# Optimization experiments

Hardware: AMD Instinct MI355X
Metric: run time of the kernel (lower is better)

## Reference

```python
import jax, jax.numpy as jnp
import numpy as np

NEG_INF = -1e30  # log-domain 'zero' (avoid -inf for numerical safety)


def ctc_loss(labels, logits, label_length, logit_length, blank_index=0):
    """Per-example CTC negative log-likelihood.

    labels:       [B, L] int, dense, padded (values != blank within label_length)
    logits:       [T, B, V] float, time-major (TF ctc_loss_v2 default)
    label_length: [B] int
    logit_length: [B] int
    returns:      [B] float, -log p(labels | logits)
    """
    T, B, V = logits.shape
    L = labels.shape[1]
    S = 2 * L + 1  # extended label sequence: blank, l1, blank, l2, ..., blank

    logp = jax.nn.log_softmax(logits, axis=-1)  # [T, B, V]

    # Extended label sequence per batch element: ext[:, 0::2] = blank, ext[:, 1::2] = labels
    ext = jnp.full((B, S), blank_index, dtype=labels.dtype)
    ext = ext.at[:, 1::2].set(labels)  # [B, S]

    # Emission log-probs for each extended position: emit[t, b, s] = logp[t, b, ext[b, s]]
    emit = jnp.take_along_axis(
        logp, jnp.broadcast_to(ext[None].astype(jnp.int32), (T, B, S)), axis=2
    )  # [T, B, S]

    # Skip transition s-2 -> s allowed iff ext[s] != blank and ext[s] != ext[s-2]
    ext_m2 = jnp.concatenate(
        [jnp.full((B, 2), -1, dtype=labels.dtype), ext[:, :-2]], axis=1
    )
    skip_ok = (ext != blank_index) & (ext != ext_m2)  # [B, S]

    def shift(a, k):
        # shift right along S by k, filling with NEG_INF
        return jnp.concatenate(
            [jnp.full((B, k), NEG_INF, dtype=a.dtype), a[:, :-k]], axis=1
        )

    # alpha at t=0: only positions 0 (blank) and 1 (first label) are reachable
    alpha0 = jnp.full((B, S), NEG_INF, dtype=logits.dtype)
    alpha0 = alpha0.at[:, 0].set(emit[0, :, 0]).at[:, 1].set(emit[0, :, 1])

    def step(alpha, xs):
        emit_t, t = xs  # emit_t: [B, S], t: scalar time index
        cand = jnp.stack(
            [alpha, shift(alpha, 1), jnp.where(skip_ok, shift(alpha, 2), NEG_INF)],
            axis=0,
        )  # [3, B, S]
        new = jax.nn.logsumexp(cand, axis=0) + emit_t
        # Freeze alpha for samples whose logit sequence has ended
        new = jnp.where((t < logit_length)[:, None], new, alpha)
        return new, None

    ts = jnp.arange(1, T)
    alpha, _ = jax.lax.scan(step, alpha0, (emit[1:], ts))  # [B, S]

    b = jnp.arange(B)
    end = 2 * label_length  # index of trailing blank for each sample
    ll = jnp.logaddexp(alpha[b, end], alpha[b, jnp.maximum(end - 1, 0)])
    return -ll  # [B]


def setup_inputs() -> dict:
    key = jax.random.key(0)
    k1, k2, k3 = jax.random.split(key, 3)
    T, B, V, L = 1024, 64, 256, 256
    logits = jax.random.normal(k1, (T, B, V), dtype=jnp.float32)
    # labels avoid the blank index (0)
    labels = jax.random.randint(k2, (B, L), 1, V, dtype=jnp.int32)
    label_length = jax.random.randint(k3, (B,), L // 2, L + 1, dtype=jnp.int32)
    logit_length = jnp.full((B,), T, dtype=jnp.int32)
    return {
        "labels": labels,
        "logits": logits,
        "label_length": label_length,
        "logit_length": logit_length,
    }


def reference(labels, logits, label_length, logit_length):
    # CTCLossEndpointCpu: loss = reduce_mean(ctc_loss_v2(...)) with blank_index=0
    per_example = ctc_loss(labels, logits, label_length, logit_length, blank_index=0)
    return jnp.mean(per_example)
```

## Files before the change

### kernel.cpp

```cpp
#include <hip/hip_runtime.h>
#include <math.h>


constexpr int V = 256;
constexpr float LN2_F = 0.6931471805599453f;

typedef unsigned uint2v __attribute__((ext_vector_type(2)));

template <int CTRL>
__device__ __forceinline__ float dpp_mov_f(float x) {
    return __int_as_float(__builtin_amdgcn_update_dpp(
        0, __float_as_int(x), CTRL, 0xF, 0xF, true));
}

__device__ __forceinline__ float wave_shr1_f(float x) {
    return __int_as_float(__builtin_amdgcn_update_dpp(
        0, __float_as_int(x), 0x138, 0xF, 0xF, true));
}

__device__ __forceinline__ float wave_max_f(float m) {
    m = fmaxf(m, dpp_mov_f<0xB1>(m));
    m = fmaxf(m, dpp_mov_f<0x4E>(m));
    m = fmaxf(m, dpp_mov_f<0x124>(m));
    m = fmaxf(m, dpp_mov_f<0x128>(m));
#if __has_builtin(__builtin_amdgcn_permlane16_swap) && __has_builtin(__builtin_amdgcn_permlane32_swap)
    uint2v a = __builtin_amdgcn_permlane16_swap(__float_as_uint(m),
                                                __float_as_uint(m), false, false);
    m = fmaxf(__uint_as_float(a.x), __uint_as_float(a.y));
    uint2v b = __builtin_amdgcn_permlane32_swap(__float_as_uint(m),
                                                __float_as_uint(m), false, false);
    m = fmaxf(__uint_as_float(b.x), __uint_as_float(b.y));
#else
    m = fmaxf(m, __shfl_xor(m, 16, 64));
    m = fmaxf(m, __shfl_xor(m, 32, 64));
#endif
    return m;
}

__device__ __forceinline__ float wave_sum_f(float s) {
    s += dpp_mov_f<0xB1>(s);
    s += dpp_mov_f<0x4E>(s);
    s += dpp_mov_f<0x124>(s);
    s += dpp_mov_f<0x128>(s);
#if __has_builtin(__builtin_amdgcn_permlane16_swap) && __has_builtin(__builtin_amdgcn_permlane32_swap)
    uint2v a = __builtin_amdgcn_permlane16_swap(__float_as_uint(s),
                                                __float_as_uint(s), false, false);
    s = __uint_as_float(a.x) + __uint_as_float(a.y);
    uint2v b = __builtin_amdgcn_permlane32_swap(__float_as_uint(s),
                                                __float_as_uint(s), false, false);
    s = __uint_as_float(b.x) + __uint_as_float(b.y);
#else
    s += __shfl_xor(s, 16, 64);
    s += __shfl_xor(s, 32, 64);
#endif
    return s;
}

#define MACS(EB, E1, E3, E5, E7) do {                                  \
    const float c7m = wave_shr1_f(cur7);                               \
    curT = (curT + cur7) * (EB);                                       \
    cur7 = fmaf(sk7, cur5, cur7 + cur6) * (E7);                        \
    cur6 = (cur6 + cur5) * (EB);                                       \
    cur5 = fmaf(sk5, cur3, cur5 + cur4) * (E5);                        \
    cur4 = (cur4 + cur3) * (EB);                                       \
    cur3 = fmaf(sk3, cur1, cur3 + cur2) * (E3);                        \
    cur2 = (cur2 + cur1) * (EB);                                       \
    cur1 = fmaf(sk1, c7m, cur1 + cur0) * (E1);                         \
    cur0 = (cur0 + c7m) * (EB);                                        \
  } while (0)

#define RENORM do {                                                    \
    curT *= mkT; cur0 *= mk0; cur1 *= mk1; cur2 *= mk2; cur3 *= mk3;   \
    cur4 *= mk4; cur5 *= mk5; cur6 *= mk6; cur7 *= mk7;                \
    float _m = fmaxf(curT, cur0); _m = fmaxf(_m, cur1);                \
    _m = fmaxf(_m, cur2); _m = fmaxf(_m, cur3); _m = fmaxf(_m, cur4);  \
    _m = fmaxf(_m, cur5); _m = fmaxf(_m, cur6); _m = fmaxf(_m, cur7);  \
    _m = wave_max_f(_m);                                               \
    const float _inv = 1.f / fmaxf(_m, 1e-30f);                        \
    log2acc -= log2f(_inv);                                            \
    curT *= _inv; cur0 *= _inv; cur1 *= _inv; cur2 *= _inv;            \
    cur3 *= _inv; cur4 *= _inv; cur5 *= _inv; cur6 *= _inv;            \
    cur7 *= _inv;                                                      \
  } while (0)

#define PRE(N, S) do {                                                 \
    G##N = *(const float4*)(&gbuf[h][S][l][0]);                        \
    A##N = bbuf[h][S];                                                 \
  } while (0)
#define STEPR(N, S) do {                                               \
    MACS(A##N, G##N.x, G##N.y, G##N.z, G##N.w);                        \
    PRE(N, S);                                                         \
  } while (0)
#define STEPC(N) MACS(A##N, G##N.x, G##N.y, G##N.z, G##N.w)

#define PLOAD(dst, WV, J)                                              \
    dst = *(const float4*)(lg + rs * (size_t)(16 * (WV) + p + 7 * (J)) + 4 * l)
#define PROC(XV, i) do {                                               \
    float4 _e;                                                         \
    _e.x = __expf((XV).x); _e.y = __expf((XV).y);                      \
    _e.z = __expf((XV).z); _e.w = __expf((XV).w);                      \
    *(float4*)&prow[p][4 * l] = _e;                                    \
    const float* _pr = prow[p];                                        \
    float _gb = _pr[0];                                                \
    float4 _gv;                                                        \
    _gv.x = _pr[ix]; _gv.y = _pr[iy]; _gv.z = _pr[iz]; _gv.w = _pr[iw];\
    *(float4*)&gbuf[h][i][l][0] = _gv;                                 \
    if (l == 0) bbuf[h][i] = _gb;                                      \
  } while (0)

#define WG_BARRIER asm volatile("s_waitcnt lgkmcnt(0)\n\ts_barrier" ::: "memory")

__global__ __launch_bounds__(512) void ctc_main(
    const int*   __restrict__ labels,
    const float* __restrict__ logits,
    const int*   __restrict__ label_len,
    const int*   __restrict__ logit_len,
    float*       __restrict__ partial,
    float*       __restrict__ lnterm,
    int T, int B, int L)
{
    const int tid = threadIdx.x;
    const int wid = tid >> 6;
    const int l   = tid & 63;

    if ((int)blockIdx.x < B) {
        __shared__ __align__(16) float gbuf[2][16][64][4];
        __shared__ float bbuf[2][16];
        __shared__ __align__(16) float prow[7][256];
        __shared__ float afin[514];

        const int b = blockIdx.x;
        const int Tb = logit_len[b];
        const int Lb = label_len[b];
        const int Sb = 2 * Lb + 1;

        const float* lg = logits + (size_t)b * V;
        const size_t rs = (size_t)B * V;

        const int4 lb4 = ((const int4*)(labels + (size_t)b * L))[l];
        const int ix = lb4.x, iy = lb4.y, iz = lb4.z, iw = lb4.w;
        const int prevw = __shfl_up(iw, 1);
        const float sk1 = (l > 0 && ix != prevw) ? 1.f : 0.f;
        const float sk3 = (iy != ix) ? 1.f : 0.f;
        const float sk5 = (iz != iy) ? 1.f : 0.f;
        const float sk7 = (iw != iz) ? 1.f : 0.f;

        const float mk0 = (8 * l + 0 < Sb) ? 1.f : 0.f;
        const float mk1 = (8 * l + 1 < Sb) ? 1.f : 0.f;
        const float mk2 = (8 * l + 2 < Sb) ? 1.f : 0.f;
        const float mk3 = (8 * l + 3 < Sb) ? 1.f : 0.f;
        const float mk4 = (8 * l + 4 < Sb) ? 1.f : 0.f;
        const float mk5 = (8 * l + 5 < Sb) ? 1.f : 0.f;
        const float mk6 = (8 * l + 6 < Sb) ? 1.f : 0.f;
        const float mk7 = (8 * l + 7 < Sb) ? 1.f : 0.f;
        const float mkT = (Sb > 512 && l == 63) ? 1.f : 0.f;

        float cur0 = 0.f, cur1 = 0.f, cur2 = 0.f, cur3 = 0.f;
        float cur4 = 0.f, cur5 = 0.f, cur6 = 0.f, cur7 = 0.f, curT = 0.f;
        if (l == 0) {
            cur0 = __expf(lg[0]);
            cur1 = __expf(lg[ix]) * mk1;
        }
        float log2acc = 0.f;

        const int NW = Tb / 16;

        float4 G0{}, G1{}, G2{}, G3{}, G4{}, G5{}, G6{}, G7{};
        float  A0 = 0, A1 = 0, A2 = 0, A3 = 0, A4 = 0, A5 = 0, A6 = 0, A7 = 0;

        const int p = (wid > 0) ? wid - 1 : 0;
        const bool three = (p < 2);
        float4 ca{}, cb{}, cc{}, na{}, nb{}, nc{};
        if (wid > 0 && NW > 0) {
            PLOAD(ca, 0, 0);
            PLOAD(cb, 0, 1);
            if (three) PLOAD(cc, 0, 2);
        }
        if (wid == 0) __builtin_amdgcn_s_setprio(1);

        for (int k = 0; k <= NW; ++k) {
            if (wid != 0) {
                if (k < NW) {
                    const int h = k & 1;
                    if (k + 1 < NW) {
                        PLOAD(na, k + 1, 0);
                        PLOAD(nb, k + 1, 1);
                        if (three) PLOAD(nc, k + 1, 2);
                    }
                    PROC(ca, p);
                    PROC(cb, p + 7);
                    if (three) PROC(cc, p + 14);
                    ca = na; cb = nb; cc = nc;
                }
            } else if (k >= 1) {
                const int w = k - 1;
                const int h = w & 1;
                if (w == 0) {
                    PRE(1, 1); PRE(2, 2); PRE(3, 3); PRE(4, 4);
                    PRE(5, 5); PRE(6, 6); PRE(7, 7); PRE(0, 8);
                    STEPR(1, 9);  STEPR(2, 10); STEPR(3, 11); STEPR(4, 12);
                    STEPR(5, 13); STEPR(6, 14); STEPR(7, 15);
                    STEPC(0);
                    STEPC(1); STEPC(2); STEPC(3); STEPC(4);
                    STEPC(5); STEPC(6); STEPC(7);
                } else {
                    PRE(0, 0); PRE(1, 1); PRE(2, 2); PRE(3, 3);
                    PRE(4, 4); PRE(5, 5); PRE(6, 6); PRE(7, 7);
                    STEPR(0, 8);  STEPR(1, 9);  STEPR(2, 10); STEPR(3, 11);
                    STEPR(4, 12); STEPR(5, 13); STEPR(6, 14); STEPR(7, 15);
                    STEPC(0); STEPC(1); STEPC(2); STEPC(3);
                    STEPC(4); STEPC(5); STEPC(6); STEPC(7);
                }
                RENORM;
            }
            WG_BARRIER;
        }

        if (wid == 0) {
            for (int t = 16 * NW; t < Tb; ++t) {
                if (t < 1) continue;
                const float* rowp = lg + rs * (size_t)t;
                const float eb = __expf(rowp[0]);
                const float e1 = __expf(rowp[ix]), e3 = __expf(rowp[iy]);
                const float e5 = __expf(rowp[iz]), e7 = __expf(rowp[iw]);
                MACS(eb, e1, e3, e5, e7);
            }

            afin[8 * l + 0] = cur0; afin[8 * l + 1] = cur1;
            afin[8 * l + 2] = cur2; afin[8 * l + 3] = cur3;
            afin[8 * l + 4] = cur4; afin[8 * l + 5] = cur5;
            afin[8 * l + 6] = cur6; afin[8 * l + 7] = cur7;
            if (l == 63) afin[512] = curT;
            const int end = 2 * Lb;
            const int em1 = (end > 0) ? end - 1 : 0;
            float ssum = afin[end] + afin[em1];
            ssum = fmaxf(ssum, 1e-37f);
            if (l == 0) lnterm[b] = logf(ssum) + LN2_F * log2acc;
        }
    } else {
        const int w  = ((int)blockIdx.x - B) * 8 + wid;
        const int nW = ((int)gridDim.x - B) * 8;
        const int rows = T * B;
        const int bb = w % B;
        const int Tbb = logit_len[bb];
        float acc = 0.f;
        int r = w;
        if (r < rows) {
            int t = w / B;
            const int ts = nW / B;
            float4 nxt = ((const float4*)(logits + (size_t)r * V))[l];
            while (true) {
                const int rn = r + nW;
                const bool more = rn < rows;
                const float4 x = nxt;
                if (more) nxt = ((const float4*)(logits + (size_t)rn * V))[l];
                float m = fmaxf(fmaxf(x.x, x.y), fmaxf(x.z, x.w));
                m = wave_max_f(m);
                float ss = __expf(x.x - m) + __expf(x.y - m) +
                           __expf(x.z - m) + __expf(x.w - m);
                ss = wave_sum_f(ss);
                if (t < Tbb) acc += m + logf(ss);
                if (!more) break;
                r = rn; t += ts;
            }
        }
        if (l == 0) partial[w] = acc;
    }
}

__global__ __launch_bounds__(64) void ctc_final(
    const float* __restrict__ partial,
    const float* __restrict__ lnterm,
    float* __restrict__ out, int B, int nW)
{
    const int b = threadIdx.x;
    float v = 0.f;
    if (b < B) {
        float c = 0.f;
        for (int k = b; k < nW; k += B) c += partial[k];
        v = c - lnterm[b];
    }
    #pragma unroll
    for (int o = 32; o >= 1; o >>= 1) v += __shfl_xor(v, o, 64);
    if (threadIdx.x == 0) out[0] = v / (float)B;
}

extern "C" void kernel_launch(void* const* d_in, const int* in_sizes, int n_in,
                              void* d_out, int out_size, void* d_ws, size_t ws_size,
                              hipStream_t stream) {
    const int*   labels    = (const int*)d_in[0];
    const float* logits    = (const float*)d_in[1];
    const int*   label_len = (const int*)d_in[2];
    const int*   logit_len = (const int*)d_in[3];

    const int B = in_sizes[2];
    const int L = in_sizes[0] / B;
    const int T = in_sizes[1] / (B * V);

    const int nLse = 1024;
    float* partial = (float*)d_ws;
    float* lnterm  = partial + nLse;

    ctc_main<<<B + nLse / 8, 512, 0, stream>>>(labels, logits, label_len,
                                               logit_len, partial, lnterm,
                                               T, B, L);
    ctc_final<<<1, 64, 0, stream>>>(partial, lnterm, (float*)d_out, B, nLse);
}
```

Before: 165.2 us.

## Split CTC into pre-gather/LSE kernel and streamlined recursion kernel

Adds a first kernel that computes per-row log-sum-exp partials and gathers exp(logit) values for each sample's labels into a contiguous workspace buffer. A second 64-thread-per-sample kernel then runs the alpha recursion, streaming from that compact buffer with deep register prefetch. It also folds the final mean into the recursion kernel using an atomic counter, removing the separate final kernel. This relies on a large workspace, with the old fused path kept as a fallback, and it adds an extra global write and read of the gathered data.

Measured after the change: 224.1 us. 35.7% more time.

```diff
diff --git a/kernel.cpp b/kernel.cpp
--- a/kernel.cpp
+++ b/kernel.cpp
@@ -82,6 +82,218 @@
     cur3 *= _inv; cur4 *= _inv; cur5 *= _inv; cur6 *= _inv;            \
     cur7 *= _inv;                                                      \
   } while (0)
+
+__global__ __launch_bounds__(256) void ctc_gather_lse(
+    const int*   __restrict__ labels,
+    const float* __restrict__ logits,
+    const int*   __restrict__ logit_len,
+    float*       __restrict__ partial,
+    float*       __restrict__ ggath,
+    float*       __restrict__ bgath,
+    int*         __restrict__ cnt,
+    int T, int B, int L)
+{
+    const int wid = threadIdx.x >> 6;
+    const int l   = threadIdx.x & 63;
+    if (blockIdx.x == 0 && threadIdx.x == 0) cnt[0] = 0;
+
+    __shared__ __align__(16) float erow[4][256];
+    float* er = erow[wid];
+
+    const int w  = (int)blockIdx.x * 4 + wid;
+    const int nW = (int)gridDim.x * 4;
+    const int rows = T * B;
+    const int bb = w % B;
+    const int Tbb = logit_len[bb];
+
+    const int4 lb4 = ((const int4*)(labels + (size_t)bb * L))[l];
+    const int ix = lb4.x, iy = lb4.y, iz = lb4.z, iw = lb4.w;
+
+    float acc = 0.f;
+    int r = w;
+    if (r < rows) {
+        int t = w / B;
+        const int ts = nW / B;
+        float4 nxt = ((const float4*)(logits + (size_t)r * V))[l];
+        while (true) {
+            const int rn = r + nW;
+            const bool more = rn < rows;
+            const float4 x = nxt;
+            if (more) nxt = ((const float4*)(logits + (size_t)rn * V))[l];
+            float4 e4;
+            e4.x = __expf(x.x); e4.y = __expf(x.y);
+            e4.z = __expf(x.z); e4.w = __expf(x.w);
+            ((float4*)er)[l] = e4;
+            float m = fmaxf(fmaxf(x.x, x.y), fmaxf(x.z, x.w));
+            m = wave_max_f(m);
+            float ss = __expf(x.x - m) + __expf(x.y - m) +
+                       __expf(x.z - m) + __expf(x.w - m);
+            ss = wave_sum_f(ss);
+            float4 g;
+            g.x = er[ix]; g.y = er[iy]; g.z = er[iz]; g.w = er[iw];
+            const float gb0 = er[0];
+            float* gr = ggath + ((size_t)bb * T + t) * 256;
+            ((float4*)gr)[l] = g;
+            if (l == 0) bgath[(size_t)bb * T + t] = gb0;
+            if (t < Tbb) acc += m + logf(ss);
+            if (!more) break;
+            r = rn; t += ts;
+        }
+    }
+    if (l == 0) partial[w] = acc;
+}
+
+#define GROWC(TROW) (*(const float4*)(gb + 256 * (size_t)((TROW) > Tm1 ? Tm1 : (TROW)) + 4 * l))
+#define BROWC(TROW) (*(const float4*)(bb_ + ((TROW) > Tm4 ? Tm4 : (TROW))))
+
+#define KSTEP(TT, SL, ABL) do {                                        \
+    MACS((ABL), R##SL.x, R##SL.y, R##SL.z, R##SL.w);                   \
+    R##SL = GROWC((TT) + 16);                                          \
+  } while (0)
+
+#define WIN16(BASE, K0, K1, K2, K3) do {                               \
+    KSTEP((BASE) +  0,  0, (K0).x); KSTEP((BASE) +  1,  1, (K0).y);    \
+    KSTEP((BASE) +  2,  2, (K0).z); KSTEP((BASE) +  3,  3, (K0).w);    \
+    K0 = BROWC((BASE) + 32);                                           \
+    KSTEP((BASE) +  4,  4, (K1).x); KSTEP((BASE) +  5,  5, (K1).y);    \
+    KSTEP((BASE) +  6,  6, (K1).z); KSTEP((BASE) +  7,  7, (K1).w);    \
+    K1 = BROWC((BASE) + 36);                                           \
+    KSTEP((BASE) +  8,  8, (K2).x); KSTEP((BASE) +  9,  9, (K2).y);    \
+    KSTEP((BASE) + 10, 10, (K2).z); KSTEP((BASE) + 11, 11, (K2).w);    \
+    K2 = BROWC((BASE) + 40);                                           \
+    KSTEP((BASE) + 12, 12, (K3).x); KSTEP((BASE) + 13, 13, (K3).y);    \
+    KSTEP((BASE) + 14, 14, (K3).z); KSTEP((BASE) + 15, 15, (K3).w);    \
+    K3 = BROWC((BASE) + 44);                                           \
+    RENORM;                                                            \
+  } while (0)
+
+#define W0FIRST() do {                                                 \
+    KSTEP( 1,  1, blkA0.y); KSTEP( 2,  2, blkA0.z); KSTEP( 3,  3, blkA0.w); \
+    blkA0 = BROWC(32);                                                 \
+    KSTEP( 4,  4, blkA1.x); KSTEP( 5,  5, blkA1.y);                    \
+    KSTEP( 6,  6, blkA1.z); KSTEP( 7,  7, blkA1.w);                    \
+    blkA1 = BROWC(36);                                                 \
+    KSTEP( 8,  8, blkA2.x); KSTEP( 9,  9, blkA2.y);                    \
+    KSTEP(10, 10, blkA2.z); KSTEP(11, 11, blkA2.w);                    \
+    blkA2 = BROWC(40);                                                 \
+    KSTEP(12, 12, blkA3.x); KSTEP(13, 13, blkA3.y);                    \
+    KSTEP(14, 14, blkA3.z); KSTEP(15, 15, blkA3.w);                    \
+    blkA3 = BROWC(44);                                                 \
+    RENORM;                                                            \
+  } while (0)
+
+__global__ __launch_bounds__(64) void ctc_rec(
+    const int*   __restrict__ labels,
+    const float* __restrict__ logits,
+    const int*   __restrict__ label_len,
+    const int*   __restrict__ logit_len,
+    const float* __restrict__ partial,
+    const float* __restrict__ ggath,
+    const float* __restrict__ bgath,
+    float*       __restrict__ vbuf,
+    int*         __restrict__ cnt,
+    float*       __restrict__ out,
+    int T, int B, int L, int nLse)
+{
+    const int l = threadIdx.x;
+    const int b = blockIdx.x;
+    __shared__ float afin[514];
+
+    const int Tb = logit_len[b];
+    const int Lb = label_len[b];
+    const int Sb = 2 * Lb + 1;
+    const int Tm1 = T - 1;
+    const int Tm4 = T - 4;
+
+    const float* lg  = logits + (size_t)b * V;
+    const size_t rs  = (size_t)B * V;
+    const float* gb  = ggath + (size_t)b * T * 256;
+    const float* bb_ = bgath + (size_t)b * T;
+
+    const int4 lb4 = ((const int4*)(labels + (size_t)b * L))[l];
+    const int ix = lb4.x, iy = lb4.y, iz = lb4.z, iw = lb4.w;
+    const int prevw = __shfl_up(iw, 1);
+    const float sk1 = (l > 0 && ix != prevw) ? 1.f : 0.f;
+    const float sk3 = (iy != ix) ? 1.f : 0.f;
+    const float sk5 = (iz != iy) ? 1.f : 0.f;
+    const float sk7 = (iw != iz) ? 1.f : 0.f;
+
+    const float mk0 = (8 * l + 0 < Sb) ? 1.f : 0.f;
+    const float mk1 = (8 * l + 1 < Sb) ? 1.f : 0.f;
+    const float mk2 = (8 * l + 2 < Sb) ? 1.f : 0.f;
+    const float mk3 = (8 * l + 3 < Sb) ? 1.f : 0.f;
+    const float mk4 = (8 * l + 4 < Sb) ? 1.f : 0.f;
+    const float mk5 = (8 * l + 5 < Sb) ? 1.f : 0.f;
+    const float mk6 = (8 * l + 6 < Sb) ? 1.f : 0.f;
+    const float mk7 = (8 * l + 7 < Sb) ? 1.f : 0.f;
+    const float mkT = (Sb > 512 && l == 63) ? 1.f : 0.f;
+
+    float cur0 = 0.f, cur1 = 0.f, cur2 = 0.f, cur3 = 0.f;
+    float cur4 = 0.f, cur5 = 0.f, cur6 = 0.f, cur7 = 0.f, curT = 0.f;
+    if (l == 0) {
+        cur0 = __expf(lg[0]);
+        cur1 = __expf(lg[ix]) * mk1;
+    }
+    float log2acc = 0.f;
+
+    int base = 1;
+    if (Tb >= 16) {
+        float4 R0, R1, R2, R3, R4, R5, R6, R7;
+        float4 R8, R9, R10, R11, R12, R13, R14, R15;
+        R1  = GROWC(1);  R2  = GROWC(2);  R3  = GROWC(3);  R4  = GROWC(4);
+        R5  = GROWC(5);  R6  = GROWC(6);  R7  = GROWC(7);  R8  = GROWC(8);
+        R9  = GROWC(9);  R10 = GROWC(10); R11 = GROWC(11); R12 = GROWC(12);
+        R13 = GROWC(13); R14 = GROWC(14); R15 = GROWC(15); R0  = GROWC(16);
+        float4 blkA0 = BROWC(0),  blkA1 = BROWC(4);
+        float4 blkA2 = BROWC(8),  blkA3 = BROWC(12);
+        float4 blkB0 = BROWC(16), blkB1 = BROWC(20);
+        float4 blkB2 = BROWC(24), blkB3 = BROWC(28);
+
+        W0FIRST();
+        int wv = 1;
+        for (base = 16; base + 16 <= Tb; base += 16, ++wv) {
+            if (wv & 1) WIN16(base, blkB0, blkB1, blkB2, blkB3);
+            else        WIN16(base, blkA0, blkA1, blkA2, blkA3);
+        }
+    }
+    for (int t = base; t < Tb; ++t) {
+        const float* rowp = lg + rs * (size_t)t;
+        const float eb = __expf(rowp[0]);
+        const float e1 = __expf(rowp[ix]), e3 = __expf(rowp[iy]);
+        const float e5 = __expf(rowp[iz]), e7 = __expf(rowp[iw]);
+        MACS(eb, e1, e3, e5, e7);
+    }
+
+    afin[8 * l + 0] = cur0; afin[8 * l + 1] = cur1;
+    afin[8 * l + 2] = cur2; afin[8 * l + 3] = cur3;
+    afin[8 * l + 4] = cur4; afin[8 * l + 5] = cur5;
+    afin[8 * l + 6] = cur6; afin[8 * l + 7] = cur7;
+    if (l == 63) afin[512] = curT;
+    const int end = 2 * Lb;
+    const int em1 = (end > 0) ? end - 1 : 0;
+    float ssum = afin[end] + afin[em1];
+    ssum = fmaxf(ssum, 1e-37f);
+    const float lnt = logf(ssum) + LN2_F * log2acc;
+
+    float c = 0.f;
+    for (int k = b; k < nLse; k += B) c += partial[k];
+    const float v = c - lnt;
+
+    int old = 0;
+    if (l == 0) {
+        atomicExch(&vbuf[b], v);
+        __threadfence();
+        old = atomicAdd(cnt, 1);
+    }
+    old = __shfl(old, 0, 64);
+    if (old == B - 1) {
+        __threadfence();
+        float vv = atomicAdd(&vbuf[l], 0.0f);
+        #pragma unroll
+        for (int o = 32; o >= 1; o >>= 1) vv += __shfl_xor(vv, o, 64);
+        if (l == 0) out[0] = vv / (float)B;
+    }
+}
 
 #define PRE(N, S) do {                                                 \
     G##N = *(const float4*)(&gbuf[h][S][l][0]);                        \
@@ -298,11 +510,30 @@
     const int T = in_sizes[1] / (B * V);
 
     const int nLse = 1024;
-    float* partial = (float*)d_ws;
-    float* lnterm  = partial + nLse;
-
-    ctc_main<<<B + nLse / 8, 512, 0, stream>>>(labels, logits, label_len,
-                                               logit_len, partial, lnterm,
-                                               T, B, L);
-    ctc_final<<<1, 64, 0, stream>>>(partial, lnterm, (float*)d_out, B, nLse);
-}
+
+    const size_t ggathN = (size_t)B * T * 256;
+    const size_t bgathN = (size_t)B * T;
+    const size_t need   = (ggathN + bgathN + nLse + B + 16) * sizeof(float);
+
+    if (ws_size >= need) {
+        float* ggath   = (float*)d_ws;
+        float* bgath   = ggath + ggathN;
+        float* partial = bgath + bgathN;
+        float* vbuf    = partial + nLse;
+        int*   cnt     = (int*)(vbuf + B);
+
+        ctc_gather_lse<<<256, 256, 0, stream>>>(labels, logits, logit_len,
+                                                partial, ggath, bgath, cnt,
+                                                T, B, L);
+        ctc_rec<<<B, 64, 0, stream>>>(labels, logits, label_len, logit_len,
+                                      partial, ggath, bgath, vbuf, cnt,
+                                      (float*)d_out, T, B, L, nLse);
+    } else {
+        float* partial = (float*)d_ws;
+        float* lnterm  = partial + nLse;
+        ctc_main<<<B + nLse / 8, 512, 0, stream>>>(labels, logits, label_len,
+                                                   logit_len, partial, lnterm,
+                                                   T, B, L);
+        ctc_final<<<1, 64, 0, stream>>>(partial, lnterm, (float*)d_out, B, nLse);
+    }
+}
```

## Fuse log-softmax normalizer into per-sample CTC block with 1024-thread producers

Applied to the files above, without the earlier changes.

Replaces the split design, where extra blocks computed the per-row log-sum-exp normalizers, with one 1024-thread block per sample. In that block, 15 producer waves exponentiate the logit rows into a double-buffered shared row buffer and also accumulate the per-row log-sum-exp. The alpha-recursion wave now gathers label emissions directly from the full exponentiated rows instead of pre-gathered buffers, and the prefetch distance grows to two windows. This removes the redundant second read of logits by separate LSE blocks, but it leaves only B blocks and specializes on the test shape, with the old kernel kept as a fallback.

Measured after the change: 174.4 us. 1.06x slower.

```diff
diff --git a/kernel.cpp b/kernel.cpp
--- a/kernel.cpp
+++ b/kernel.cpp
@@ -83,59 +83,49 @@
     cur7 *= _inv;                                                      \
   } while (0)
 
+#define DECLSET(N) float g##N##a = 0, g##N##b = 0, g##N##c = 0,        \
+                         g##N##d = 0, g##N##e = 0
 #define PRE(N, S) do {                                                 \
-    G##N = *(const float4*)(&gbuf[h][S][l][0]);                        \
-    A##N = bbuf[h][S];                                                 \
+    const float* _er = er + 256 * (S);                                 \
+    g##N##a = _er[ix]; g##N##b = _er[iy];                              \
+    g##N##c = _er[iz]; g##N##d = _er[iw];                              \
+    g##N##e = _er[0];                                                  \
   } while (0)
 #define STEPR(N, S) do {                                               \
-    MACS(A##N, G##N.x, G##N.y, G##N.z, G##N.w);                        \
+    MACS(g##N##e, g##N##a, g##N##b, g##N##c, g##N##d);                 \
     PRE(N, S);                                                         \
   } while (0)
-#define STEPC(N) MACS(A##N, G##N.x, G##N.y, G##N.z, G##N.w)
-
-#define PLOAD(dst, WV, J)                                              \
-    dst = *(const float4*)(lg + rs * (size_t)(16 * (WV) + p + 7 * (J)) + 4 * l)
-#define PROC(XV, i) do {                                               \
-    float4 _e;                                                         \
-    _e.x = __expf((XV).x); _e.y = __expf((XV).y);                      \
-    _e.z = __expf((XV).z); _e.w = __expf((XV).w);                      \
-    *(float4*)&prow[p][4 * l] = _e;                                    \
-    const float* _pr = prow[p];                                        \
-    float _gb = _pr[0];                                                \
-    float4 _gv;                                                        \
-    _gv.x = _pr[ix]; _gv.y = _pr[iy]; _gv.z = _pr[iz]; _gv.w = _pr[iw];\
-    *(float4*)&gbuf[h][i][l][0] = _gv;                                 \
-    if (l == 0) bbuf[h][i] = _gb;                                      \
-  } while (0)
+#define STEPC(N) MACS(g##N##e, g##N##a, g##N##b, g##N##c, g##N##d)
 
 #define WG_BARRIER asm volatile("s_waitcnt lgkmcnt(0)\n\ts_barrier" ::: "memory")
 
-__global__ __launch_bounds__(512) void ctc_main(
+__global__ __launch_bounds__(1024) void ctc_main(
     const int*   __restrict__ labels,
     const float* __restrict__ logits,
     const int*   __restrict__ label_len,
     const int*   __restrict__ logit_len,
-    float*       __restrict__ partial,
-    float*       __restrict__ lnterm,
+    float*       __restrict__ vres,
     int T, int B, int L)
 {
     const int tid = threadIdx.x;
     const int wid = tid >> 6;
     const int l   = tid & 63;
-
-    if ((int)blockIdx.x < B) {
-        __shared__ __align__(16) float gbuf[2][16][64][4];
-        __shared__ float bbuf[2][16];
-        __shared__ __align__(16) float prow[7][256];
-        __shared__ float afin[514];
-
-        const int b = blockIdx.x;
-        const int Tb = logit_len[b];
-        const int Lb = label_len[b];
+    const int b   = blockIdx.x;
+
+    __shared__ __align__(16) float erow[2][16][256];
+    __shared__ float afin[514];
+    __shared__ float accbuf[16];
+
+    const int Tb = logit_len[b];
+    const int Lb = label_len[b];
+    const int NW = Tb / 16;
+
+    const float* lg = logits + (size_t)b * V;
+    const size_t rs = (size_t)B * V;
+
+    if (wid == 0) {
+        __builtin_amdgcn_s_setprio(1);
         const int Sb = 2 * Lb + 1;
-
-        const float* lg = logits + (size_t)b * V;
-        const size_t rs = (size_t)B * V;
 
         const int4 lb4 = ((const int4*)(labels + (size_t)b * L))[l];
         const int ix = lb4.x, iy = lb4.y, iz = lb4.z, iw = lb4.w;
@@ -163,38 +153,13 @@
         }
         float log2acc = 0.f;
 
-        const int NW = Tb / 16;
-
-        float4 G0{}, G1{}, G2{}, G3{}, G4{}, G5{}, G6{}, G7{};
-        float  A0 = 0, A1 = 0, A2 = 0, A3 = 0, A4 = 0, A5 = 0, A6 = 0, A7 = 0;
-
-        const int p = (wid > 0) ? wid - 1 : 0;
-        const bool three = (p < 2);
-        float4 ca{}, cb{}, cc{}, na{}, nb{}, nc{};
-        if (wid > 0 && NW > 0) {
-            PLOAD(ca, 0, 0);
-            PLOAD(cb, 0, 1);
-            if (three) PLOAD(cc, 0, 2);
-        }
-        if (wid == 0) __builtin_amdgcn_s_setprio(1);
+        DECLSET(0); DECLSET(1); DECLSET(2); DECLSET(3);
+        DECLSET(4); DECLSET(5); DECLSET(6); DECLSET(7);
 
         for (int k = 0; k <= NW; ++k) {
-            if (wid != 0) {
-                if (k < NW) {
-                    const int h = k & 1;
-                    if (k + 1 < NW) {
-                        PLOAD(na, k + 1, 0);
-                        PLOAD(nb, k + 1, 1);
-                        if (three) PLOAD(nc, k + 1, 2);
-                    }
-                    PROC(ca, p);
-                    PROC(cb, p + 7);
-                    if (three) PROC(cc, p + 14);
-                    ca = na; cb = nb; cc = nc;
-                }
-            } else if (k >= 1) {
+            if (k >= 1) {
                 const int w = k - 1;
-                const int h = w & 1;
+                const float* er = &erow[w & 1][0][0];
                 if (w == 0) {
                     PRE(1, 1); PRE(2, 2); PRE(3, 3); PRE(4, 4);
                     PRE(5, 5); PRE(6, 6); PRE(7, 7); PRE(0, 8);
@@ -210,6 +175,265 @@
                     STEPR(4, 12); STEPR(5, 13); STEPR(6, 14); STEPR(7, 15);
                     STEPC(0); STEPC(1); STEPC(2); STEPC(3);
                     STEPC(4); STEPC(5); STEPC(6); STEPC(7);
+                }
+                RENORM;
+            }
+            WG_BARRIER;
+        }
+
+        for (int t = 16 * NW; t < Tb; ++t) {
+            if (t < 1) continue;
+            const float* rowp = lg + rs * (size_t)t;
+            const float eb = __expf(rowp[0]);
+            const float e1 = __expf(rowp[ix]), e3 = __expf(rowp[iy]);
+            const float e5 = __expf(rowp[iz]), e7 = __expf(rowp[iw]);
+            MACS(eb, e1, e3, e5, e7);
+        }
+
+        afin[8 * l + 0] = cur0; afin[8 * l + 1] = cur1;
+        afin[8 * l + 2] = cur2; afin[8 * l + 3] = cur3;
+        afin[8 * l + 4] = cur4; afin[8 * l + 5] = cur5;
+        afin[8 * l + 6] = cur6; afin[8 * l + 7] = cur7;
+        if (l == 63) afin[512] = curT;
+        const int end = 2 * Lb;
+        const int em1 = (end > 0) ? end - 1 : 0;
+        float ssum = afin[end] + afin[em1];
+        ssum = fmaxf(ssum, 1e-37f);
+        const float lnt = logf(ssum) + LN2_F * log2acc;
+
+        WG_BARRIER;
+
+        float c = 0.f;
+        #pragma unroll
+        for (int q = 0; q < 16; ++q) c += accbuf[q];
+        if (l == 0) vres[b] = c - lnt;
+    } else {
+        const int s0   = wid - 1;
+        const bool dual = (wid == 15);
+        float accA = 0.f, accB = 0.f;
+
+        float4 pc0{}, pn0{}, pc1{}, pn1{};
+        if (NW > 0) {
+            pc0 = *(const float4*)(lg + rs * (size_t)s0 + 4 * l);
+            pn0 = *(const float4*)(lg + rs * (size_t)(16 + s0) + 4 * l);
+            if (dual) {
+                pc1 = *(const float4*)(lg + rs * (size_t)15 + 4 * l);
+                pn1 = *(const float4*)(lg + rs * (size_t)31 + 4 * l);
+            }
+        }
+
+        for (int k = 0; k <= NW; ++k) {
+            if (k < NW) {
+                const int hh = k & 1;
+                const float4 x0 = pc0;
+                pc0 = pn0;
+                if (k + 2 < NW)
+                    pn0 = *(const float4*)(lg + rs * (size_t)(16 * (k + 2) + s0) + 4 * l);
+                float4 x1{};
+                if (dual) {
+                    x1 = pc1;
+                    pc1 = pn1;
+                    if (k + 2 < NW)
+                        pn1 = *(const float4*)(lg + rs * (size_t)(16 * (k + 2) + 15) + 4 * l);
+                }
+                float4 e0;
+                e0.x = __expf(x0.x); e0.y = __expf(x0.y);
+                e0.z = __expf(x0.z); e0.w = __expf(x0.w);
+                *(float4*)&erow[hh][s0][4 * l] = e0;
+                if (dual) {
+                    float4 e1v;
+                    e1v.x = __expf(x1.x); e1v.y = __expf(x1.y);
+                    e1v.z = __expf(x1.z); e1v.w = __expf(x1.w);
+                    *(float4*)&erow[hh][15][4 * l] = e1v;
+                }
+                {
+                    float m = fmaxf(fmaxf(x0.x, x0.y), fmaxf(x0.z, x0.w));
+                    m = wave_max_f(m);
+                    float ss = __expf(x0.x - m) + __expf(x0.y - m) +
+                               __expf(x0.z - m) + __expf(x0.w - m);
+                    ss = wave_sum_f(ss);
+                    const int t = 16 * k + s0;
+                    if (t < Tb) accA += m + logf(ss);
+                }
+                if (dual) {
+                    float m = fmaxf(fmaxf(x1.x, x1.y), fmaxf(x1.z, x1.w));
+                    m = wave_max_f(m);
+                    float ss = __expf(x1.x - m) + __expf(x1.y - m) +
+                               __expf(x1.z - m) + __expf(x1.w - m);
+                    ss = wave_sum_f(ss);
+                    const int t = 16 * k + 15;
+                    if (t < Tb) accB += m + logf(ss);
+                }
+            }
+            WG_BARRIER;
+        }
+
+        for (int t = 16 * NW + s0; t < Tb; t += 16) {
+            const float4 x = *(const float4*)(lg + rs * (size_t)t + 4 * l);
+            float m = fmaxf(fmaxf(x.x, x.y), fmaxf(x.z, x.w));
+            m = wave_max_f(m);
+            float ss = __expf(x.x - m) + __expf(x.y - m) +
+                       __expf(x.z - m) + __expf(x.w - m);
+            ss = wave_sum_f(ss);
+            accA += m + logf(ss);
+        }
+        if (dual) {
+            for (int t = 16 * NW + 15; t < Tb; t += 16) {
+                const float4 x = *(const float4*)(lg + rs * (size_t)t + 4 * l);
+                float m = fmaxf(fmaxf(x.x, x.y), fmaxf(x.z, x.w));
+                m = wave_max_f(m);
+                float ss = __expf(x.x - m) + __expf(x.y - m) +
+                           __expf(x.z - m) + __expf(x.w - m);
+                ss = wave_sum_f(ss);
+                accB += m + logf(ss);
+            }
+        }
+        if (l == 0) {
+            accbuf[s0] = accA;
+            if (dual) accbuf[15] = accB;
+        }
+        WG_BARRIER;
+    }
+}
+
+__global__ __launch_bounds__(64) void ctc_final(
+    const float* __restrict__ vres,
+    float* __restrict__ out, int B)
+{
+    const int b = threadIdx.x;
+    float v = (b < B) ? vres[b] : 0.f;
+    #pragma unroll
+    for (int o = 32; o >= 1; o >>= 1) v += __shfl_xor(v, o, 64);
+    if (threadIdx.x == 0) out[0] = v / (float)B;
+}
+
+#define FB_PRE(N, S) do {                                              \
+    G##N = *(const float4*)(&gbuf[h][S][l][0]);                        \
+    A##N = bbuf[h][S];                                                 \
+  } while (0)
+#define FB_STEPR(N, S) do {                                            \
+    MACS(A##N, G##N.x, G##N.y, G##N.z, G##N.w);                        \
+    FB_PRE(N, S);                                                      \
+  } while (0)
+#define FB_STEPC(N) MACS(A##N, G##N.x, G##N.y, G##N.z, G##N.w)
+
+#define FB_PLOAD(dst, WV, J)                                           \
+    dst = *(const float4*)(lg + rs * (size_t)(16 * (WV) + p + 7 * (J)) + 4 * l)
+#define FB_PROC(XV, i) do {                                            \
+    float4 _e;                                                         \
+    _e.x = __expf((XV).x); _e.y = __expf((XV).y);                      \
+    _e.z = __expf((XV).z); _e.w = __expf((XV).w);                      \
+    *(float4*)&prow[p][4 * l] = _e;                                    \
+    const float* _pr = prow[p];                                        \
+    float _gb = _pr[0];                                                \
+    float4 _gv;                                                        \
+    _gv.x = _pr[ix]; _gv.y = _pr[iy]; _gv.z = _pr[iz]; _gv.w = _pr[iw];\
+    *(float4*)&gbuf[h][i][l][0] = _gv;                                 \
+    if (l == 0) bbuf[h][i] = _gb;                                      \
+  } while (0)
+
+__global__ __launch_bounds__(512) void fb_ctc_main(
+    const int*   __restrict__ labels,
+    const float* __restrict__ logits,
+    const int*   __restrict__ label_len,
+    const int*   __restrict__ logit_len,
+    float*       __restrict__ partial,
+    float*       __restrict__ lnterm,
+    int T, int B, int L)
+{
+    const int tid = threadIdx.x;
+    const int wid = tid >> 6;
+    const int l   = tid & 63;
+
+    if ((int)blockIdx.x < B) {
+        __shared__ __align__(16) float gbuf[2][16][64][4];
+        __shared__ float bbuf[2][16];
+        __shared__ __align__(16) float prow[7][256];
+        __shared__ float afin[514];
+
+        const int b = blockIdx.x;
+        const int Tb = logit_len[b];
+        const int Lb = label_len[b];
+        const int Sb = 2 * Lb + 1;
+
+        const float* lg = logits + (size_t)b * V;
+        const size_t rs = (size_t)B * V;
+
+        const int4 lb4 = ((const int4*)(labels + (size_t)b * L))[l];
+        const int ix = lb4.x, iy = lb4.y, iz = lb4.z, iw = lb4.w;
+        const int prevw = __shfl_up(iw, 1);
+        const float sk1 = (l > 0 && ix != prevw) ? 1.f : 0.f;
+        const float sk3 = (iy != ix) ? 1.f : 0.f;
+        const float sk5 = (iz != iy) ? 1.f : 0.f;
+        const float sk7 = (iw != iz) ? 1.f : 0.f;
+
+        const float mk0 = (8 * l + 0 < Sb) ? 1.f : 0.f;
+        const float mk1 = (8 * l + 1 < Sb) ? 1.f : 0.f;
+        const float mk2 = (8 * l + 2 < Sb) ? 1.f : 0.f;
+        const float mk3 = (8 * l + 3 < Sb) ? 1.f : 0.f;
+        const float mk4 = (8 * l + 4 < Sb) ? 1.f : 0.f;
+        const float mk5 = (8 * l + 5 < Sb) ? 1.f : 0.f;
+        const float mk6 = (8 * l + 6 < Sb) ? 1.f : 0.f;
+        const float mk7 = (8 * l + 7 < Sb) ? 1.f : 0.f;
+        const float mkT = (Sb > 512 && l == 63) ? 1.f : 0.f;
+
+        float cur0 = 0.f, cur1 = 0.f, cur2 = 0.f, cur3 = 0.f;
+        float cur4 = 0.f, cur5 = 0.f, cur6 = 0.f, cur7 = 0.f, curT = 0.f;
+        if (l == 0) {
+            cur0 = __expf(lg[0]);
+            cur1 = __expf(lg[ix]) * mk1;
+        }
+        float log2acc = 0.f;
+
+        const int NW = Tb / 16;
+
+        float4 G0{}, G1{}, G2{}, G3{}, G4{}, G5{}, G6{}, G7{};
+        float  A0 = 0, A1 = 0, A2 = 0, A3 = 0, A4 = 0, A5 = 0, A6 = 0, A7 = 0;
+
+        const int p = (wid > 0) ? wid - 1 : 0;
+        const bool three = (p < 2);
+        float4 ca{}, cb{}, cc{}, na{}, nb{}, nc{};
+        if (wid > 0 && NW > 0) {
+            FB_PLOAD(ca, 0, 0);
+            FB_PLOAD(cb, 0, 1);
+            if (three) FB_PLOAD(cc, 0, 2);
+        }
+        if (wid == 0) __builtin_amdgcn_s_setprio(1);
+
+        for (int k = 0; k <= NW; ++k) {
+            if (wid != 0) {
+                if (k < NW) {
+                    const int h = k & 1;
+                    if (k + 1 < NW) {
+                        FB_PLOAD(na, k + 1, 0);
+                        FB_PLOAD(nb, k + 1, 1);
+                        if (three) FB_PLOAD(nc, k + 1, 2);
+                    }
+                    FB_PROC(ca, p);
+                    FB_PROC(cb, p + 7);
+                    if (three) FB_PROC(cc, p + 14);
+                    ca = na; cb = nb; cc = nc;
+                }
+            } else if (k >= 1) {
+                const int w = k - 1;
+                const int h = w & 1;
+                if (w == 0) {
+                    FB_PRE(1, 1); FB_PRE(2, 2); FB_PRE(3, 3); FB_PRE(4, 4);
+                    FB_PRE(5, 5); FB_PRE(6, 6); FB_PRE(7, 7); FB_PRE(0, 8);
+                    FB_STEPR(1, 9);  FB_STEPR(2, 10); FB_STEPR(3, 11);
+                    FB_STEPR(4, 12); FB_STEPR(5, 13); FB_STEPR(6, 14);
+                    FB_STEPR(7, 15);
+                    FB_STEPC(0);
+                    FB_STEPC(1); FB_STEPC(2); FB_STEPC(3); FB_STEPC(4);
+                    FB_STEPC(5); FB_STEPC(6); FB_STEPC(7);
+                } else {
+                    FB_PRE(0, 0); FB_PRE(1, 1); FB_PRE(2, 2); FB_PRE(3, 3);
+                    FB_PRE(4, 4); FB_PRE(5, 5); FB_PRE(6, 6); FB_PRE(7, 7);
+                    FB_STEPR(0, 8);  FB_STEPR(1, 9);  FB_STEPR(2, 10);
+                    FB_STEPR(3, 11); FB_STEPR(4, 12); FB_STEPR(5, 13);
+                    FB_STEPR(6, 14); FB_STEPR(7, 15);
+                    FB_STEPC(0); FB_STEPC(1); FB_STEPC(2); FB_STEPC(3);
+                    FB_STEPC(4); FB_STEPC(5); FB_STEPC(6); FB_STEPC(7);
                 }
                 RENORM;
             }
@@ -268,7 +492,7 @@
     }
 }
 
-__global__ __launch_bounds__(64) void ctc_final(
+__global__ __launch_bounds__(64) void fb_ctc_final(
     const float* __restrict__ partial,
     const float* __restrict__ lnterm,
     float* __restrict__ out, int B, int nW)
@@ -297,12 +521,20 @@
     const int L = in_sizes[0] / B;
     const int T = in_sizes[1] / (B * V);
 
-    const int nLse = 1024;
-    float* partial = (float*)d_ws;
-    float* lnterm  = partial + nLse;
-
-    ctc_main<<<B + nLse / 8, 512, 0, stream>>>(labels, logits, label_len,
-                                               logit_len, partial, lnterm,
-                                               T, B, L);
-    ctc_final<<<1, 64, 0, stream>>>(partial, lnterm, (float*)d_out, B, nLse);
-}
+    if (T == 1024 && B == 64 && L == 256 && ws_size >= (size_t)B * sizeof(float)) {
+        float* vres = (float*)d_ws;
+        ctc_main<<<B, 1024, 0, stream>>>(labels, logits, label_len, logit_len,
+                                         vres, T, B, L);
+        ctc_final<<<1, 64, 0, stream>>>(vres, (float*)d_out, B);
+    } else {
+        const int nLse = 1024;
+        float* partial = (float*)d_ws;
+        float* lnterm  = partial + nLse;
+        fb_ctc_main<<<B + nLse / 8, 512, 0, stream>>>(labels, logits,
+                                                      label_len, logit_len,
+                                                      partial, lnterm,
+                                                      T, B, L);
+        fb_ctc_final<<<1, 64, 0, stream>>>(partial, lnterm, (float*)d_out,
+                                           B, nLse);
+    }
+}
```
